# Kernel tuning notes

Measured on AMD Instinct MI355X. Metric: run time of the kernel, lower is better.

## Reference

```python
import jax, jax.numpy as jnp
import numpy as np

N, D, H, K = 50000, 384, 128, 16
WALK_STEPS = 3
EPS = 1e-8


def setup_inputs() -> dict:
    key = jax.random.key(0)
    ks = jax.random.split(key, 7)
    emb = jax.random.normal(ks[0], (N, D), dtype=jnp.float32)
    qv = jax.random.normal(ks[1], (D,), dtype=jnp.float32)
    W1 = jax.random.normal(ks[2], (2 * D, H), dtype=jnp.float32) * (1.0 / np.sqrt(2 * D))
    b1 = jax.random.normal(ks[3], (H,), dtype=jnp.float32) * 0.01
    W2 = jax.random.normal(ks[4], (H, K), dtype=jnp.float32) * (1.0 / np.sqrt(H))
    b2 = jax.random.normal(ks[5], (K,), dtype=jnp.float32) * 0.01
    nbr = jax.random.randint(ks[6], (N, K), 0, N, dtype=jnp.int64)
    return {"emb": emb, "qv": qv, "W1": W1, "b1": b1, "W2": W2, "b2": b2, "nbr": nbr}


def reference(emb, qv, W1, b1, W2, b2, nbr):
    n, k = nbr.shape
    # Per-node coin: coin_net(concat(emb_i, qv)) -> normalized rank-1 outer product.
    # (Coin does not depend on the walk state, so compute once; original recomputes
    # the identical values every step.)
    inp = jnp.concatenate([emb, jnp.broadcast_to(qv, (n, qv.shape[0]))], axis=-1)  # [n, 2d]
    h = jax.nn.relu(inp @ W1 + b1)                                                 # [n, H]
    amps = h @ W2 + b2                                                             # [n, k]
    amps = amps / (jnp.linalg.norm(amps, axis=-1, keepdims=True) + EPS)
    coin = amps[:, :, None] * amps[:, None, :]                                     # [n, k, k]
    fro = jnp.linalg.norm(coin.reshape(n, -1), axis=-1)[:, None, None]
    coin = coin / (fro + EPS)
    # Reverse-slot lookup: for edge slot (i, idx) with j = nbr[i, idx], find first p
    # with nbr[j, p] == i (the .index(i) in the original); missing -> dropped.
    match = nbr[nbr] == jnp.arange(n, dtype=nbr.dtype)[:, None, None]              # [n, k, k]
    rev_idx = jnp.argmax(match, axis=-1)                                           # [n, k]
    rev_mask = jnp.any(match, axis=-1)                                             # [n, k]
    flat_tgt = (nbr * k + rev_idx).reshape(-1)
    # Initial state is real and the coin is real (cast to cfloat in the original),
    # so the walk state stays real-valued; |z|^2 == z^2 here.
    state = jnp.full((n, k), 1.0 / np.sqrt(n * k), dtype=emb.dtype)

    def step(state, _):
        s_p = jnp.einsum('nij,nj->ni', coin, state)                                # coin @ state
        contrib = jnp.where(rev_mask, s_p, 0.0)
        new = jnp.zeros(n * k, dtype=state.dtype).at[flat_tgt].add(contrib.reshape(-1))
        new = new.reshape(n, k)
        new = new / (jnp.sqrt(jnp.sum(new * new)) + EPS)
        return new, None

    state, _ = jax.lax.scan(step, state, None, length=WALK_STEPS)
    probs = jnp.sum(state * state, axis=1)
    return jnp.nan_to_num(probs, nan=0.0, posinf=1.0, neginf=0.0)
```

## Files before the change

### kernel.cpp

```cpp
#include <hip/hip_runtime.h>
#include <math.h>

#define N_NODES 50000
#define DIM     384
#define HID     128
#define KN      16
#define NK      (N_NODES * KN)
#define EPSF    1e-8f

#define NSLAB   1563
#define SLABCAP 8
#define CAPR2   1024
#define BT2     1024

#define OFF_CNT   1024u
#define OFF_ET    8192u
#define OFF_R4    108544u

__global__ __launch_bounds__(512)
void scan_coin_kernel(const int* __restrict__ nbr, const float* __restrict__ emb,
                      const float* __restrict__ qv, const float* __restrict__ W1,
                      const float* __restrict__ b1, const float* __restrict__ W2,
                      const float* __restrict__ b2,
                      int* __restrict__ cnt, int2* __restrict__ slab_et,
                      float4* __restrict__ rec4,
                      float* __restrict__ out) {
    __shared__ int   wcnt[8];
    __shared__ int   recE[SLABCAP];
    __shared__ int   recT[SLABCAP];
    __shared__ float sq[DIM];
    __shared__ float prt[4 * HID];
    __shared__ float c1s[HID];
    __shared__ float sh[HID];
    __shared__ float prt2[32 * KN];
    __shared__ float samps[KN];

    int b = blockIdx.x, tid = threadIdx.x;
    int e = b * 512 + tid;
    if (e < N_NODES) out[e] = 0.f;

    bool valid = (e < NK);
    int ecl = valid ? e : 0;
    int j = nbr[ecl];
    const int4* rp = (const int4*)(nbr + (size_t)j * KN);
    int4 r0 = rp[0], r1 = rp[1], r2 = rp[2], r3 = rp[3];
    int i = ecl >> 4;
    unsigned m = 0;
    m |= (unsigned)(r0.x == i) << 0;  m |= (unsigned)(r0.y == i) << 1;
    m |= (unsigned)(r0.z == i) << 2;  m |= (unsigned)(r0.w == i) << 3;
    m |= (unsigned)(r1.x == i) << 4;  m |= (unsigned)(r1.y == i) << 5;
    m |= (unsigned)(r1.z == i) << 6;  m |= (unsigned)(r1.w == i) << 7;
    m |= (unsigned)(r2.x == i) << 8;  m |= (unsigned)(r2.y == i) << 9;
    m |= (unsigned)(r2.z == i) << 10; m |= (unsigned)(r2.w == i) << 11;
    m |= (unsigned)(r3.x == i) << 12; m |= (unsigned)(r3.y == i) << 13;
    m |= (unsigned)(r3.z == i) << 14; m |= (unsigned)(r3.w == i) << 15;
    bool flag = valid && (m != 0);
    int p = __ffs(m) - 1;

    unsigned long long bal = __ballot(flag);
    int lane = tid & 63, w = tid >> 6;
    if (lane == 0) wcnt[w] = __popcll(bal);
    __syncthreads();
    int wb = 0, tot = 0;
    #pragma unroll
    for (int x = 0; x < 8; ++x) { int v = wcnt[x]; tot += v; if (x < w) wb += v; }
    int tot_ = (tot > SLABCAP) ? SLABCAP : tot;
    if (tid == 0) cnt[b] = tot_;
    if (flag) {
        int rank = wb + __popcll(bal & ((1ull << lane) - 1ull));
        if (rank < SLABCAP) { recE[rank] = e; recT[rank] = j * KN + p; }
    }
    if (tot_ == 0) return;
    __syncthreads();
    if (tid < tot_)
        slab_et[b * SLABCAP + tid] = make_int2(recE[tid], recT[tid]);

    if (tid < DIM) sq[tid] = qv[tid];
    __syncthreads();
    int c = tid & 127, g = tid >> 7;
    {
        const float* wp = W1 + (size_t)(DIM + g * 96) * HID + c;
        float acc = 0.f;
        #pragma unroll 16
        for (int d = 0; d < 96; ++d)
            acc += sq[g * 96 + d] * wp[(size_t)d * HID];
        prt[g * HID + c] = acc;
    }
    __syncthreads();
    if (tid < HID)
        c1s[tid] = b1[tid] + prt[tid] + prt[HID + tid] + prt[2 * HID + tid] + prt[3 * HID + tid];

    for (int q = 0; q < tot_; ++q) {
        int e2 = recE[q];
        int node = e2 >> 4;
        __syncthreads();
        if (tid < DIM) sq[tid] = emb[(size_t)node * DIM + tid];
        __syncthreads();
        const float* wp = W1 + (size_t)(g * 96) * HID + c;
        float acc = 0.f;
        #pragma unroll 16
        for (int d = 0; d < 96; ++d)
            acc += sq[g * 96 + d] * wp[(size_t)d * HID];
        prt[g * HID + c] = acc;
        __syncthreads();
        if (tid < HID)
            sh[tid] = fmaxf(c1s[tid] + prt[tid] + prt[HID + tid]
                            + prt[2 * HID + tid] + prt[3 * HID + tid], 0.f);
        __syncthreads();
        int k = tid & 15, g2 = tid >> 4;
        float a2 = 0.f;
        #pragma unroll
        for (int jj = 0; jj < 4; ++jj)
            a2 += sh[g2 * 4 + jj] * W2[(size_t)(g2 * 4 + jj) * KN + k];
        prt2[g2 * KN + k] = a2;
        __syncthreads();
        if (tid < KN) {
            float s = b2[tid];
            #pragma unroll
            for (int g3 = 0; g3 < 32; ++g3) s += prt2[g3 * KN + tid];
            samps[tid] = s;
        }
        __syncthreads();
        if (tid == 0) {
            float ss = 0.f;
            #pragma unroll
            for (int t2 = 0; t2 < KN; ++t2) ss += samps[t2] * samps[t2];
            float inv_na = 1.f / (sqrtf(ss) + EPSF);
            float fro = 0.f, sa = 0.f;
            #pragma unroll
            for (int t2 = 0; t2 < KN; ++t2) {
                float av = samps[t2] * inv_na;
                fro += av * av; sa += av;
            }
            float av_src = samps[e2 & 15] * inv_na;
            float invf = 1.f / (fro + EPSF);
            rec4[b * SLABCAP + q] = make_float4(av_src, av_src * invf, sa, 0.f);
        }
    }
}

__global__ __launch_bounds__(BT2)
void walk_kernel(const int* __restrict__ cnt, const int2* __restrict__ slab_et,
                 const float4* __restrict__ rec4, float* __restrict__ out) {
    __shared__ int   baseL[2048];
    __shared__ int   cntL[2048];
    __shared__ int   erL[CAPR2];
    __shared__ int   nodeL[CAPR2];
    __shared__ int   trecL[CAPR2];
    __shared__ int   segLo[CAPR2];
    __shared__ int   segHi[CAPR2];
    __shared__ float asL[CAPR2];
    __shared__ float faL[CAPR2];
    __shared__ float d0L[CAPR2];
    __shared__ float stA[CAPR2];
    __shared__ float stB[CAPR2];
    __shared__ float dtL[CAPR2];
    __shared__ int   wsumL[16];
    __shared__ float redL[16];

    int tid = threadIdx.x;
    int lane = tid & 63, w = tid >> 6;

    int s0 = tid * 2, s1 = tid * 2 + 1;
    int lc0 = (s0 < NSLAB) ? cnt[s0] : 0;
    int lc1 = (s1 < NSLAB) ? cnt[s1] : 0;
    int ts = lc0 + lc1;
    int vinc = ts;
    #pragma unroll
    for (int off = 1; off < 64; off <<= 1) {
        int n = __shfl_up(vinc, off, 64);
        if (lane >= off) vinc += n;
    }
    if (lane == 63) wsumL[w] = vinc;
    __syncthreads();
    int wb = 0, Mtot = 0;
    #pragma unroll
    for (int x = 0; x < 16; ++x) { int v = wsumL[x]; Mtot += v; if (x < w) wb += v; }
    int base = wb + vinc - ts;
    baseL[s0] = base;       cntL[s0] = lc0;
    baseL[s1] = base + lc0; cntL[s1] = lc1;
    int M = (Mtot > CAPR2) ? CAPR2 : Mtot;
    const float S0 = 1.0f / sqrtf((float)N_NODES * (float)KN);

    for (int q = 0; q < lc0; ++q) {
        int r = base + q;
        if (r < CAPR2) {
            int2   et = slab_et[s0 * SLABCAP + q];
            float4 rc = rec4[s0 * SLABCAP + q];
            erL[r] = et.x; nodeL[r] = et.x >> 4;
            trecL[r] = et.y;
            asL[r] = rc.x; faL[r] = rc.y;
            d0L[r] = S0 * rc.z;
            stA[r] = 0.f; stB[r] = 0.f;
        }
    }
    for (int q = 0; q < lc1; ++q) {
        int r = base + lc0 + q;
        if (r < CAPR2) {
            int2   et = slab_et[s1 * SLABCAP + q];
            float4 rc = rec4[s1 * SLABCAP + q];
            erL[r] = et.x; nodeL[r] = et.x >> 4;
            trecL[r] = et.y;
            asL[r] = rc.x; faL[r] = rc.y;
            d0L[r] = S0 * rc.z;
            stA[r] = 0.f; stB[r] = 0.f;
        }
    }
    __syncthreads();

    for (int r = tid; r < M; r += BT2) {
        int t  = trecL[r];
        int bt = t >> 9;
        int bs = baseL[bt], bc = cntL[bt];
        int tr = -1;
        for (int q = 0; q < bc; ++q) {
            int r2 = bs + q;
            if (r2 < CAPR2 && erL[r2] == t) { tr = r2; break; }
        }
        trecL[r] = tr;
        int nd = nodeL[r];
        int lo = r; while (lo > 0 && nodeL[lo - 1] == nd) --lo;
        int hi = r; while (hi < M - 1 && nodeL[hi + 1] == nd) ++hi;
        segLo[r] = lo; segHi[r] = hi;
    }
    __syncthreads();

    auto NORM = [&](float* buf, float* zb) {
        float part = 0.f;
        for (int r = tid; r < M; r += BT2) part += buf[r] * buf[r];
        #pragma unroll
        for (int off = 32; off > 0; off >>= 1) part += __shfl_xor(part, off, 64);
        if (lane == 0) redL[w] = part;
        __syncthreads();
        float tot = 0.f;
        #pragma unroll
        for (int x = 0; x < 16; ++x) tot += redL[x];
        float si = 1.0f / (sqrtf(tot) + EPSF);
        for (int r = tid; r < M; r += BT2) {
            buf[r] *= si;
            if (zb) zb[r] = 0.f;
        }
        __syncthreads();
    };
    auto DOT = [&](const float* st) {
        for (int r = tid; r < M; r += BT2) {
            float d = 0.f;
            int hi = segHi[r];
            for (int r2 = segLo[r]; r2 <= hi; ++r2) d += asL[r2] * st[r2];
            dtL[r] = d;
        }
        __syncthreads();
    };

    for (int r = tid; r < M; r += BT2)
        if (trecL[r] >= 0) atomicAdd(&stA[trecL[r]], faL[r] * d0L[r]);
    __syncthreads();
    NORM(stA, d0L);

    DOT(stA);
    for (int r = tid; r < M; r += BT2)
        if (trecL[r] >= 0) atomicAdd(&stB[trecL[r]], faL[r] * dtL[r]);
    __syncthreads();
    NORM(stB, nullptr);

    DOT(stB);
    for (int r = tid; r < M; r += BT2)
        if (trecL[r] >= 0) atomicAdd(&d0L[trecL[r]], faL[r] * dtL[r]);
    __syncthreads();
    NORM(d0L, nullptr);

    for (int r = tid; r < M; r += BT2) {
        float v = d0L[r];
        atomicAdd(&out[nodeL[r]], v * v);
    }
}

extern "C" void kernel_launch(void* const* d_in, const int* in_sizes, int n_in,
                              void* d_out, int out_size, void* d_ws, size_t ws_size,
                              hipStream_t stream) {
    const float* emb = (const float*)d_in[0];
    const float* qv  = (const float*)d_in[1];
    const float* W1  = (const float*)d_in[2];
    const float* b1  = (const float*)d_in[3];
    const float* W2  = (const float*)d_in[4];
    const float* b2  = (const float*)d_in[5];
    const int*   nbr = (const int*)d_in[6];
    float*       out = (float*)d_out;

    char* ws = (char*)d_ws;
    int*    cnt     = (int*)(ws + OFF_CNT);
    int2*   slab_et = (int2*)(ws + OFF_ET);
    float4* rec4    = (float4*)(ws + OFF_R4);

    scan_coin_kernel<<<NSLAB, 512, 0, stream>>>(
        nbr, emb, qv, W1, b1, W2, b2, cnt, slab_et, rec4, out);
    walk_kernel<<<1, BT2, 0, stream>>>(cnt, slab_et, rec4, out);
}
```

Measured before the change: 30.33 us.

## Process two edges per thread in scan kernel, halving slab count

Each scan block now covers 1024 edge slots, two per thread, so there are half as many blocks and slabs (782). The walk kernel reads one slab count per thread instead of two and drops its second record-copy loop. Target slab lookup shifts by 10 instead of 9, and the scratch offsets are repacked. The goal is fewer blocks launched and a simpler prefix scan in the walk kernel. The trade-off is that a slab still holds at most 8 records but now covers twice as many edges, so overflow truncation becomes more likely.

```diff
diff --git a/kernel.cpp b/kernel.cpp
--- a/kernel.cpp
+++ b/kernel.cpp
@@ -8,14 +8,14 @@
 #define NK      (N_NODES * KN)
 #define EPSF    1e-8f
 
-#define NSLAB   1563
+#define NSLAB   782
 #define SLABCAP 8
 #define CAPR2   1024
 #define BT2     1024
 
-#define OFF_CNT   1024u
-#define OFF_ET    8192u
-#define OFF_R4    108544u
+#define OFF_CNT   0u
+#define OFF_ET    4096u
+#define OFF_R4    69632u
 
 __global__ __launch_bounds__(512)
 void scan_coin_kernel(const int* __restrict__ nbr, const float* __restrict__ emb,
@@ -25,7 +25,8 @@
                       int* __restrict__ cnt, int2* __restrict__ slab_et,
                       float4* __restrict__ rec4,
                       float* __restrict__ out) {
-    __shared__ int   wcnt[8];
+    __shared__ int   wcnt0[8];
+    __shared__ int   wcnt1[8];
     __shared__ int   recE[SLABCAP];
     __shared__ int   recT[SLABCAP];
     __shared__ float sq[DIM];
@@ -36,39 +37,65 @@
     __shared__ float samps[KN];
 
     int b = blockIdx.x, tid = threadIdx.x;
-    int e = b * 512 + tid;
-    if (e < N_NODES) out[e] = 0.f;
-
-    bool valid = (e < NK);
-    int ecl = valid ? e : 0;
-    int j = nbr[ecl];
-    const int4* rp = (const int4*)(nbr + (size_t)j * KN);
-    int4 r0 = rp[0], r1 = rp[1], r2 = rp[2], r3 = rp[3];
-    int i = ecl >> 4;
-    unsigned m = 0;
-    m |= (unsigned)(r0.x == i) << 0;  m |= (unsigned)(r0.y == i) << 1;
-    m |= (unsigned)(r0.z == i) << 2;  m |= (unsigned)(r0.w == i) << 3;
-    m |= (unsigned)(r1.x == i) << 4;  m |= (unsigned)(r1.y == i) << 5;
-    m |= (unsigned)(r1.z == i) << 6;  m |= (unsigned)(r1.w == i) << 7;
-    m |= (unsigned)(r2.x == i) << 8;  m |= (unsigned)(r2.y == i) << 9;
-    m |= (unsigned)(r2.z == i) << 10; m |= (unsigned)(r2.w == i) << 11;
-    m |= (unsigned)(r3.x == i) << 12; m |= (unsigned)(r3.y == i) << 13;
-    m |= (unsigned)(r3.z == i) << 14; m |= (unsigned)(r3.w == i) << 15;
-    bool flag = valid && (m != 0);
-    int p = __ffs(m) - 1;
-
-    unsigned long long bal = __ballot(flag);
+    int e0 = b * 1024 + tid;
+    int e1 = e0 + 512;
+    if (e0 < N_NODES) out[e0] = 0.f;
+    if (e1 < N_NODES) out[e1] = 0.f;
+
+    bool v0 = (e0 < NK), v1 = (e1 < NK);
+    int ec0 = v0 ? e0 : 0, ec1 = v1 ? e1 : 0;
+    int j0 = nbr[ec0];
+    int j1 = nbr[ec1];
+    const int4* rp0 = (const int4*)(nbr + (size_t)j0 * KN);
+    const int4* rp1 = (const int4*)(nbr + (size_t)j1 * KN);
+    int4 a0 = rp0[0], a1 = rp0[1], a2 = rp0[2], a3 = rp0[3];
+    int4 b0 = rp1[0], b1_ = rp1[1], b2_ = rp1[2], b3 = rp1[3];
+
+    int i0 = ec0 >> 4, i1 = ec1 >> 4;
+    unsigned m0 = 0, m1 = 0;
+    m0 |= (unsigned)(a0.x == i0) << 0;  m0 |= (unsigned)(a0.y == i0) << 1;
+    m0 |= (unsigned)(a0.z == i0) << 2;  m0 |= (unsigned)(a0.w == i0) << 3;
+    m0 |= (unsigned)(a1.x == i0) << 4;  m0 |= (unsigned)(a1.y == i0) << 5;
+    m0 |= (unsigned)(a1.z == i0) << 6;  m0 |= (unsigned)(a1.w == i0) << 7;
+    m0 |= (unsigned)(a2.x == i0) << 8;  m0 |= (unsigned)(a2.y == i0) << 9;
+    m0 |= (unsigned)(a2.z == i0) << 10; m0 |= (unsigned)(a2.w == i0) << 11;
+    m0 |= (unsigned)(a3.x == i0) << 12; m0 |= (unsigned)(a3.y == i0) << 13;
+    m0 |= (unsigned)(a3.z == i0) << 14; m0 |= (unsigned)(a3.w == i0) << 15;
+    m1 |= (unsigned)(b0.x == i1) << 0;  m1 |= (unsigned)(b0.y == i1) << 1;
+    m1 |= (unsigned)(b0.z == i1) << 2;  m1 |= (unsigned)(b0.w == i1) << 3;
+    m1 |= (unsigned)(b1_.x == i1) << 4; m1 |= (unsigned)(b1_.y == i1) << 5;
+    m1 |= (unsigned)(b1_.z == i1) << 6; m1 |= (unsigned)(b1_.w == i1) << 7;
+    m1 |= (unsigned)(b2_.x == i1) << 8; m1 |= (unsigned)(b2_.y == i1) << 9;
+    m1 |= (unsigned)(b2_.z == i1) << 10;m1 |= (unsigned)(b2_.w == i1) << 11;
+    m1 |= (unsigned)(b3.x == i1) << 12; m1 |= (unsigned)(b3.y == i1) << 13;
+    m1 |= (unsigned)(b3.z == i1) << 14; m1 |= (unsigned)(b3.w == i1) << 15;
+    bool f0 = v0 && (m0 != 0);
+    bool f1 = v1 && (m1 != 0);
+    int p0 = __ffs(m0) - 1;
+    int p1 = __ffs(m1) - 1;
+
+    unsigned long long bal0 = __ballot(f0);
+    unsigned long long bal1 = __ballot(f1);
     int lane = tid & 63, w = tid >> 6;
-    if (lane == 0) wcnt[w] = __popcll(bal);
-    __syncthreads();
-    int wb = 0, tot = 0;
+    if (lane == 0) { wcnt0[w] = __popcll(bal0); wcnt1[w] = __popcll(bal1); }
+    __syncthreads();
+    int wb0 = 0, wb1 = 0, tot0 = 0, tot1 = 0;
     #pragma unroll
-    for (int x = 0; x < 8; ++x) { int v = wcnt[x]; tot += v; if (x < w) wb += v; }
+    for (int x = 0; x < 8; ++x) {
+        int u0 = wcnt0[x], u1 = wcnt1[x];
+        tot0 += u0; tot1 += u1;
+        if (x < w) { wb0 += u0; wb1 += u1; }
+    }
+    int tot = tot0 + tot1;
     int tot_ = (tot > SLABCAP) ? SLABCAP : tot;
     if (tid == 0) cnt[b] = tot_;
-    if (flag) {
-        int rank = wb + __popcll(bal & ((1ull << lane) - 1ull));
-        if (rank < SLABCAP) { recE[rank] = e; recT[rank] = j * KN + p; }
+    if (f0) {
+        int rank = wb0 + __popcll(bal0 & ((1ull << lane) - 1ull));
+        if (rank < SLABCAP) { recE[rank] = e0; recT[rank] = j0 * KN + p0; }
+    }
+    if (f1) {
+        int rank = tot0 + wb1 + __popcll(bal1 & ((1ull << lane) - 1ull));
+        if (rank < SLABCAP) { recE[rank] = e1; recT[rank] = j1 * KN + p1; }
     }
     if (tot_ == 0) return;
     __syncthreads();
@@ -108,11 +135,11 @@
                             + prt[2 * HID + tid] + prt[3 * HID + tid], 0.f);
         __syncthreads();
         int k = tid & 15, g2 = tid >> 4;
-        float a2 = 0.f;
+        float a2v = 0.f;
         #pragma unroll
         for (int jj = 0; jj < 4; ++jj)
-            a2 += sh[g2 * 4 + jj] * W2[(size_t)(g2 * 4 + jj) * KN + k];
-        prt2[g2 * KN + k] = a2;
+            a2v += sh[g2 * 4 + jj] * W2[(size_t)(g2 * 4 + jj) * KN + k];
+        prt2[g2 * KN + k] = a2v;
         __syncthreads();
         if (tid < KN) {
             float s = b2[tid];
@@ -142,8 +169,8 @@
 __global__ __launch_bounds__(BT2)
 void walk_kernel(const int* __restrict__ cnt, const int2* __restrict__ slab_et,
                  const float4* __restrict__ rec4, float* __restrict__ out) {
-    __shared__ int   baseL[2048];
-    __shared__ int   cntL[2048];
+    __shared__ int   baseL[1024];
+    __shared__ int   cntL[1024];
     __shared__ int   erL[CAPR2];
     __shared__ int   nodeL[CAPR2];
     __shared__ int   trecL[CAPR2];
@@ -161,11 +188,8 @@
     int tid = threadIdx.x;
     int lane = tid & 63, w = tid >> 6;
 
-    int s0 = tid * 2, s1 = tid * 2 + 1;
-    int lc0 = (s0 < NSLAB) ? cnt[s0] : 0;
-    int lc1 = (s1 < NSLAB) ? cnt[s1] : 0;
-    int ts = lc0 + lc1;
-    int vinc = ts;
+    int lc = (tid < NSLAB) ? cnt[tid] : 0;
+    int vinc = lc;
     #pragma unroll
     for (int off = 1; off < 64; off <<= 1) {
         int n = __shfl_up(vinc, off, 64);
@@ -176,17 +200,17 @@
     int wb = 0, Mtot = 0;
     #pragma unroll
     for (int x = 0; x < 16; ++x) { int v = wsumL[x]; Mtot += v; if (x < w) wb += v; }
-    int base = wb + vinc - ts;
-    baseL[s0] = base;       cntL[s0] = lc0;
-    baseL[s1] = base + lc0; cntL[s1] = lc1;
+    int base = wb + vinc - lc;
+    baseL[tid] = base;
+    cntL[tid]  = lc;
     int M = (Mtot > CAPR2) ? CAPR2 : Mtot;
     const float S0 = 1.0f / sqrtf((float)N_NODES * (float)KN);
 
-    for (int q = 0; q < lc0; ++q) {
+    for (int q = 0; q < lc; ++q) {
         int r = base + q;
         if (r < CAPR2) {
-            int2   et = slab_et[s0 * SLABCAP + q];
-            float4 rc = rec4[s0 * SLABCAP + q];
+            int2   et = slab_et[tid * SLABCAP + q];
+            float4 rc = rec4[tid * SLABCAP + q];
             erL[r] = et.x; nodeL[r] = et.x >> 4;
             trecL[r] = et.y;
             asL[r] = rc.x; faL[r] = rc.y;
@@ -194,23 +218,11 @@
             stA[r] = 0.f; stB[r] = 0.f;
         }
     }
-    for (int q = 0; q < lc1; ++q) {
-        int r = base + lc0 + q;
-        if (r < CAPR2) {
-            int2   et = slab_et[s1 * SLABCAP + q];
-            float4 rc = rec4[s1 * SLABCAP + q];
-            erL[r] = et.x; nodeL[r] = et.x >> 4;
-            trecL[r] = et.y;
-            asL[r] = rc.x; faL[r] = rc.y;
-            d0L[r] = S0 * rc.z;
-            stA[r] = 0.f; stB[r] = 0.f;
-        }
-    }
     __syncthreads();
 
     for (int r = tid; r < M; r += BT2) {
         int t  = trecL[r];
-        int bt = t >> 9;
+        int bt = t >> 10;
         int bs = baseL[bt], bc = cntL[bt];
         int tr = -1;
         for (int q = 0; q < bc; ++q) {
```

Measured after the change: 32.29 us. +6.5%, slower.
